# Kernel optimization log

Measured on AMD Instinct MI355X. Metric: run time of the kernel, lower is better.

Reference implementation:

```python
import jax, jax.numpy as jnp
import numpy as np
import math

D_MODEL = 1024
N_HEADS = 16
D_K = D_MODEL // N_HEADS
B, L = 4, 2048


def setup_inputs() -> dict:
    key = jax.random.key(0)
    ks = jax.random.split(key, 11)
    s = 1.0 / math.sqrt(D_MODEL)
    inp = {
        "queries": jax.random.normal(ks[0], (B, L, D_MODEL), jnp.float32),
        "keys": jax.random.normal(ks[1], (B, L, D_MODEL), jnp.float32),
        "values": jax.random.normal(ks[2], (B, L, D_MODEL), jnp.float32),
        "Wq": jax.random.normal(ks[3], (D_MODEL, D_MODEL), jnp.float32) * s,
        "bq": jax.random.normal(ks[4], (D_MODEL,), jnp.float32) * s,
        "Wk": jax.random.normal(ks[5], (D_MODEL, D_MODEL), jnp.float32) * s,
        "bk": jax.random.normal(ks[6], (D_MODEL,), jnp.float32) * s,
        "Wv": jax.random.normal(ks[7], (D_MODEL, D_MODEL), jnp.float32) * s,
        "bv": jax.random.normal(ks[8], (D_MODEL,), jnp.float32) * s,
        "Wo": jax.random.normal(ks[9], (D_MODEL, D_MODEL), jnp.float32) * s,
        "bo": jax.random.normal(ks[10], (D_MODEL,), jnp.float32) * s,
    }
    return inp


def _heads(x):
    b, l, _ = x.shape
    return x.reshape(b, l, N_HEADS, D_K).transpose(0, 2, 1, 3)  # (B,H,L,Dk)


def reference(queries, keys, values, Wq, bq, Wk, bk, Wv, bv, Wo, bo):
    Q = _heads(queries @ Wq.T + bq)
    K = _heads(keys @ Wk.T + bk)
    V = _heads(values @ Wv.T + bv)
    scores = jnp.einsum("bhqd,bhkd->bhqk", Q, K) / math.sqrt(D_K)
    t = jnp.arange(L, dtype=scores.dtype)
    time_bias = -0.1 * jnp.abs(t[None, :] - t[:, None])  # (L,L)
    attn = jax.nn.softmax(scores + time_bias[None, None], axis=-1)
    out = jnp.einsum("bhqk,bhkd->bhqd", attn, V)
    out = out.transpose(0, 2, 1, 3).reshape(queries.shape[0], L, D_MODEL)
    return out @ Wo.T + bo
```

## Files before the change

kernel.cpp:

```cpp
#include <hip/hip_runtime.h>
#include <hip/hip_bf16.h>
#include <stdint.h>

typedef __bf16 bf16x8 __attribute__((ext_vector_type(8)));
typedef float f32x4 __attribute__((ext_vector_type(4)));
typedef float f32x4v __attribute__((ext_vector_type(4)));
typedef unsigned short u16x4 __attribute__((ext_vector_type(4)));

__device__ __forceinline__ uint16_t f2bf(float f){
  __bf16 h = (__bf16)f;
  return __builtin_bit_cast(uint16_t, h);
}

__device__ __forceinline__ void gld_lds16(const void* g, void* l){
  __builtin_amdgcn_global_load_lds((const __attribute__((address_space(1))) void*)g,
                                   (__attribute__((address_space(3))) void*)l, 16, 0, 0);
}

__global__ void convert2(const float* __restrict__ s1, uint16_t* __restrict__ d1, int n4_1,
                         const float* __restrict__ s2, uint16_t* __restrict__ d2, int n4_2){
  int i = blockIdx.x * blockDim.x + threadIdx.x;
  const float* s; uint16_t* d;
  if (i < n4_1) { s = s1; d = d1; }
  else { i -= n4_1; if (i >= n4_2) return; s = s2; d = d2; }
  f32x4v v = __builtin_nontemporal_load(((const f32x4v*)s) + i);
  u16x4 o;
  o.x = f2bf(v.x); o.y = f2bf(v.y); o.z = f2bf(v.z); o.w = f2bf(v.w);
  __builtin_nontemporal_store(o, ((u16x4*)d) + i);
}

__launch_bounds__(256, 2)
__global__ void gemm_bt(const uint16_t* __restrict__ A, const uint16_t* __restrict__ W,
                        const float* __restrict__ bias, void* __restrict__ out, int mode,
                        float oscale)
{
  __shared__ uint16_t As[2][128 * 64];
  __shared__ uint16_t Ws[2][128 * 64];
  const int tid = threadIdx.x;
  const int wave = tid >> 6, lane = tid & 63;
  const int g = lane >> 4, li = lane & 15;
  const int m0 = blockIdx.x * 128, n0 = blockIdx.y * 128;
  const int wr = (wave >> 1) * 64, wc = (wave & 1) * 64;

  f32x4 acc[4][4];
#pragma unroll
  for (int m = 0; m < 4; m++)
#pragma unroll
    for (int n = 0; n < 4; n++) acc[m][n] = f32x4{0.f, 0.f, 0.f, 0.f};

  const uint16_t* Asrc[4];
  const uint16_t* Wsrc[4];
  int cid[4];
#pragma unroll
  for (int j = 0; j < 4; j++) {
    cid[j] = j * 256 + tid;
    int row = cid[j] >> 3, c = cid[j] & 7;
    int sc = c ^ (row & 7);
    Asrc[j] = A + (size_t)(m0 + row) * 1024 + sc * 8;
    Wsrc[j] = W + (size_t)(n0 + row) * 1024 + sc * 8;
  }

#pragma unroll
  for (int j = 0; j < 4; j++) {
    gld_lds16(Asrc[j], (char*)As[0] + cid[j] * 16);
    gld_lds16(Wsrc[j], (char*)Ws[0] + cid[j] * 16);
  }
  __syncthreads();

  for (int t = 0; t < 16; t++) {
    const int cur = t & 1;
    if (t < 15) {
      const int k1 = (t + 1) * 64;
      const int nxt = cur ^ 1;
#pragma unroll
      for (int j = 0; j < 4; j++) {
        gld_lds16(Asrc[j] + k1, (char*)As[nxt] + cid[j] * 16);
        gld_lds16(Wsrc[j] + k1, (char*)Ws[nxt] + cid[j] * 16);
      }
    }

    const char* Ab = (const char*)As[cur];
    const char* Wb = (const char*)Ws[cur];
#pragma unroll
    for (int kh = 0; kh < 2; kh++) {
      bf16x8 a[4], bfr[4];
#pragma unroll
      for (int m = 0; m < 4; m++) {
        int row = wr + m * 16 + li;
        int ch = (kh * 4 + g) ^ (row & 7);
        a[m] = *(const bf16x8*)(Ab + row * 128 + ch * 16);
      }
#pragma unroll
      for (int n = 0; n < 4; n++) {
        int row = wc + n * 16 + li;
        int ch = (kh * 4 + g) ^ (row & 7);
        bfr[n] = *(const bf16x8*)(Wb + row * 128 + ch * 16);
      }
#pragma unroll
      for (int m = 0; m < 4; m++)
#pragma unroll
        for (int n = 0; n < 4; n++)
          acc[m][n] = __builtin_amdgcn_mfma_f32_16x16x32_bf16(a[m], bfr[n], acc[m][n], 0, 0, 0);
    }
    __syncthreads();
  }

  if (mode == 0) {
    uint16_t* O = (uint16_t*)out;
#pragma unroll
    for (int n = 0; n < 4; n++) {
      int col = n0 + wc + n * 16 + li;
      float bv = bias[col];
#pragma unroll
      for (int m = 0; m < 4; m++) {
        int row = m0 + wr + m * 16 + g * 4;
#pragma unroll
        for (int r = 0; r < 4; r++)
          __builtin_nontemporal_store(f2bf((acc[m][n][r] + bv) * oscale),
                                      &O[(size_t)(row + r) * 1024 + col]);
      }
    }
  } else if (mode == 2) {
    uint16_t* O = (uint16_t*)out;
#pragma unroll
    for (int n = 0; n < 4; n++) {
      int col = n0 + wc + n * 16 + li;
      float bv = bias[col];
#pragma unroll
      for (int m = 0; m < 4; m++) {
        int mg = m0 + wr + m * 16 + g * 4;
        int bidx = mg >> 11;
        int l = mg & 2047;
        u16x4 pk;
        pk.x = f2bf(acc[m][n][0] + bv);
        pk.y = f2bf(acc[m][n][1] + bv);
        pk.z = f2bf(acc[m][n][2] + bv);
        pk.w = f2bf(acc[m][n][3] + bv);
        __builtin_nontemporal_store(pk,
            (u16x4*)(O + ((size_t)bidx * 1024 + col) * 2048 + l));
      }
    }
  } else {
    float* O = (float*)out;
#pragma unroll
    for (int n = 0; n < 4; n++) {
      int col = n0 + wc + n * 16 + li;
      float bv = bias[col];
#pragma unroll
      for (int m = 0; m < 4; m++) {
        int row = m0 + wr + m * 16 + g * 4;
#pragma unroll
        for (int r = 0; r < 4; r++)
          __builtin_nontemporal_store(acc[m][n][r] + bv,
                                      &O[(size_t)(row + r) * 1024 + col]);
      }
    }
  }
}

__launch_bounds__(256, 2)
__global__ void flash_attn(const uint16_t* __restrict__ Qw, const uint16_t* __restrict__ Kw,
                           const uint16_t* __restrict__ Vt, uint16_t* __restrict__ Ow)
{
  __shared__ uint16_t Ks[2][64 * 64];
  __shared__ uint16_t Vs[2][64 * 64];
  __shared__ uint16_t Ps[4][16 * 64];

  const float C2 = 0.14426950408889635f;
  const float C3 = 20.1977305724455f;

  const int tid = threadIdx.x;
  const int wave = tid >> 6, lane = tid & 63;
  const int g = lane >> 4, li = lane & 15;
  const int bh = blockIdx.x;
  const int q0 = blockIdx.y * 64;
  const int b = bh >> 4, h = bh & 15;

  const uint16_t* Qp = Qw + (size_t)(b * 2048 + q0 + wave * 16 + li) * 1024 + h * 64 + g * 8;
  bf16x8 qf0 = *(const bf16x8*)Qp;
  bf16x8 qf1 = *(const bf16x8*)(Qp + 32);

  float l_r[4] = {0.f, 0.f, 0.f, 0.f};
  f32x4 o[4];
#pragma unroll
  for (int nd = 0; nd < 4; nd++) o[nd] = f32x4{0.f, 0.f, 0.f, 0.f};

  const int cid0 = tid, cid1 = 256 + tid;
  const int kr0 = cid0 >> 3, c0 = cid0 & 7;
  const int kr1 = cid1 >> 3, c1 = cid1 & 7;
  const int sc0 = c0 ^ (kr0 & 7), sc1 = c1 ^ (kr1 & 7);

  const uint16_t* Kb0 = Kw + (size_t)(b * 2048 + kr0) * 1024 + h * 64 + sc0 * 8;
  const uint16_t* Kb1 = Kw + (size_t)(b * 2048 + kr1) * 1024 + h * 64 + sc1 * 8;
  const uint16_t* Vb0 = Vt + (size_t)(bh * 64 + kr0) * 2048 + sc0 * 8;
  const uint16_t* Vb1 = Vt + (size_t)(bh * 64 + kr1) * 2048 + sc1 * 8;

  const int kv_lo = (q0 >= 256) ? (q0 - 256) : 0;
  const int kv_hi = (q0 + 320 <= 2048) ? (q0 + 320) : 2048;
  const int ntiles = (kv_hi - kv_lo) >> 6;
  const int tq0 = q0 + wave * 16 + g * 4;

  {
    const int kv0 = kv_lo;
    gld_lds16(Kb0 + (size_t)kv0 * 1024, (char*)Ks[0] + cid0 * 16);
    gld_lds16(Kb1 + (size_t)kv0 * 1024, (char*)Ks[0] + cid1 * 16);
    gld_lds16(Vb0 + kv0, (char*)Vs[0] + cid0 * 16);
    gld_lds16(Vb1 + kv0, (char*)Vs[0] + cid1 * 16);
  }

  for (int it = 0; it < ntiles; ++it) {
    __syncthreads();
    const int cur = it & 1;
    if (it + 1 < ntiles) {
      const int kvn = kv_lo + (it + 1) * 64;
      const int nxt = cur ^ 1;
      gld_lds16(Kb0 + (size_t)kvn * 1024, (char*)Ks[nxt] + cid0 * 16);
      gld_lds16(Kb1 + (size_t)kvn * 1024, (char*)Ks[nxt] + cid1 * 16);
      gld_lds16(Vb0 + kvn, (char*)Vs[nxt] + cid0 * 16);
      gld_lds16(Vb1 + kvn, (char*)Vs[nxt] + cid1 * 16);
    }
    const int kv0 = kv_lo + it * 64;

    float p[4][4];
#pragma unroll
    for (int n = 0; n < 4; n++) {
      int kr = n * 16 + li;
      bf16x8 bk0 = *(const bf16x8*)((const char*)Ks[cur] + kr * 128 + ((g ^ (kr & 7)) << 4));
      bf16x8 bk1 = *(const bf16x8*)((const char*)Ks[cur] + kr * 128 + (((4 + g) ^ (kr & 7)) << 4));
      f32x4 s = f32x4{0.f, 0.f, 0.f, 0.f};
      s = __builtin_amdgcn_mfma_f32_16x16x32_bf16(qf0, bk0, s, 0, 0, 0);
      s = __builtin_amdgcn_mfma_f32_16x16x32_bf16(qf1, bk1, s, 0, 0, 0);
      float dtb = (float)(tq0 - (kv0 + n * 16 + li));
#pragma unroll
      for (int r = 0; r < 4; r++) {
        float e = exp2f((s[r] - C3) - C2 * fabsf(dtb + (float)r));
        p[n][r] = e;
        l_r[r] += e;
      }
    }

#pragma unroll
    for (int n = 0; n < 4; n++)
#pragma unroll
      for (int r = 0; r < 4; r++) {
        int prow = g * 4 + r;
        int c = n * 16 + li;
        Ps[wave][prow * 64 + ((((c >> 3) ^ (prow & 7))) << 3) + (c & 7)] = f2bf(p[n][r]);
      }

    bf16x8 pa0 = *(const bf16x8*)((const char*)Ps[wave] + li * 128 + ((g ^ (li & 7)) << 4));
    bf16x8 pa1 = *(const bf16x8*)((const char*)Ps[wave] + li * 128 + (((4 + g) ^ (li & 7)) << 4));
#pragma unroll
    for (int nd = 0; nd < 4; nd++) {
      int vr = nd * 16 + li;
      bf16x8 vb0 = *(const bf16x8*)((const char*)Vs[cur] + vr * 128 + ((g ^ (vr & 7)) << 4));
      bf16x8 vb1 = *(const bf16x8*)((const char*)Vs[cur] + vr * 128 + (((4 + g) ^ (vr & 7)) << 4));
      o[nd] = __builtin_amdgcn_mfma_f32_16x16x32_bf16(pa0, vb0, o[nd], 0, 0, 0);
      o[nd] = __builtin_amdgcn_mfma_f32_16x16x32_bf16(pa1, vb1, o[nd], 0, 0, 0);
    }
  }

#pragma unroll
  for (int r = 0; r < 4; r++) {
    float l = l_r[r];
    l += __shfl_xor(l, 1);
    l += __shfl_xor(l, 2);
    l += __shfl_xor(l, 4);
    l += __shfl_xor(l, 8);
    float inv = 1.0f / l;
    int qg = b * 2048 + q0 + wave * 16 + g * 4 + r;
#pragma unroll
    for (int nd = 0; nd < 4; nd++)
      __builtin_nontemporal_store(f2bf(o[nd][r] * inv),
                                  &Ow[(size_t)qg * 1024 + h * 64 + nd * 16 + li]);
  }
}

extern "C" void kernel_launch(void* const* d_in, const int* in_sizes, int n_in,
                              void* d_out, int out_size, void* d_ws, size_t ws_size,
                              hipStream_t stream) {
  const float* q  = (const float*)d_in[0];
  const float* k  = (const float*)d_in[1];
  const float* v  = (const float*)d_in[2];
  const float* Wq = (const float*)d_in[3];
  const float* bq = (const float*)d_in[4];
  const float* Wk = (const float*)d_in[5];
  const float* bk = (const float*)d_in[6];
  const float* Wv = (const float*)d_in[7];
  const float* bv = (const float*)d_in[8];
  const float* Wo = (const float*)d_in[9];
  const float* bo = (const float*)d_in[10];

  const size_t NX = (size_t)8192 * 1024;
  const size_t NW = (size_t)1024 * 1024;

  uint16_t* Xb  = (uint16_t*)d_ws;
  uint16_t* Wb  = Xb + NX;
  uint16_t* Vtw = Wb + NW;
  uint16_t* Aws = Xb;
  uint16_t* Qws = (uint16_t*)d_out;
  uint16_t* Kws = Qws + NX;

  const int n4x = (int)(NX / 4);
  const int n4w = (int)(NW / 4);
  const int gcv = (n4x + n4w) / 256;

  dim3 ggrid(64, 8);
  const float qscale = 0.18033688011112042f;

  convert2<<<gcv, 256, 0, stream>>>(q, Xb, n4x, Wq, Wb, n4w);
  gemm_bt<<<ggrid, 256, 0, stream>>>(Xb, Wb, bq, Qws, 0, qscale);

  convert2<<<gcv, 256, 0, stream>>>(k, Xb, n4x, Wk, Wb, n4w);
  gemm_bt<<<ggrid, 256, 0, stream>>>(Xb, Wb, bk, Kws, 0, 1.0f);

  convert2<<<gcv, 256, 0, stream>>>(v, Xb, n4x, Wv, Wb, n4w);
  gemm_bt<<<ggrid, 256, 0, stream>>>(Xb, Wb, bv, Vtw, 2, 1.0f);

  flash_attn<<<dim3(64, 32), 256, 0, stream>>>(Qws, Kws, Vtw, Aws);

  convert2<<<n4w / 256, 256, 0, stream>>>(Wo, Wb, n4w, (const float*)0, (uint16_t*)0, 0);
  gemm_bt<<<ggrid, 256, 0, stream>>>(Aws, Wb, bo, d_out, 3, 1.0f);
}
```

Before: 346.3 us.

## Transpose QK^T MFMA and pass P via lane shuffles instead of LDS

The flash attention kernel swaps the QK^T MFMA operands so each lane holds scores for one query row. It packs the exp'd probabilities into bf16 pairs and assembles the PV A-operand with cross-lane shuffles, removing the per-wave Ps shared-memory round trip. The row-sum reduction is restructured to match. Separately, nontemporal loads and stores are replaced with plain ones across the convert, GEMM and attention kernels. Shuffles add ds_bpermute traffic in exchange for dropping LDS writes and reads.

```diff
diff --git a/kernel.cpp b/kernel.cpp
--- a/kernel.cpp
+++ b/kernel.cpp
@@ -4,12 +4,14 @@
 
 typedef __bf16 bf16x8 __attribute__((ext_vector_type(8)));
 typedef float f32x4 __attribute__((ext_vector_type(4)));
-typedef float f32x4v __attribute__((ext_vector_type(4)));
-typedef unsigned short u16x4 __attribute__((ext_vector_type(4)));
+typedef uint32_t u32x4 __attribute__((ext_vector_type(4)));
 
 __device__ __forceinline__ uint16_t f2bf(float f){
   __bf16 h = (__bf16)f;
   return __builtin_bit_cast(uint16_t, h);
+}
+__device__ __forceinline__ uint32_t pkbf(float lo, float hi){
+  return (uint32_t)f2bf(lo) | ((uint32_t)f2bf(hi) << 16);
 }
 
 __device__ __forceinline__ void gld_lds16(const void* g, void* l){
@@ -23,10 +25,10 @@
   const float* s; uint16_t* d;
   if (i < n4_1) { s = s1; d = d1; }
   else { i -= n4_1; if (i >= n4_2) return; s = s2; d = d2; }
-  f32x4v v = __builtin_nontemporal_load(((const f32x4v*)s) + i);
-  u16x4 o;
+  float4 v = ((const float4*)s)[i];
+  ushort4 o;
   o.x = f2bf(v.x); o.y = f2bf(v.y); o.z = f2bf(v.z); o.w = f2bf(v.w);
-  __builtin_nontemporal_store(o, ((u16x4*)d) + i);
+  ((ushort4*)d)[i] = o;
 }
 
 __launch_bounds__(256, 2)
@@ -116,8 +118,7 @@
         int row = m0 + wr + m * 16 + g * 4;
 #pragma unroll
         for (int r = 0; r < 4; r++)
-          __builtin_nontemporal_store(f2bf((acc[m][n][r] + bv) * oscale),
-                                      &O[(size_t)(row + r) * 1024 + col]);
+          O[(size_t)(row + r) * 1024 + col] = f2bf((acc[m][n][r] + bv) * oscale);
       }
     }
   } else if (mode == 2) {
@@ -131,13 +132,12 @@
         int mg = m0 + wr + m * 16 + g * 4;
         int bidx = mg >> 11;
         int l = mg & 2047;
-        u16x4 pk;
+        ushort4 pk;
         pk.x = f2bf(acc[m][n][0] + bv);
         pk.y = f2bf(acc[m][n][1] + bv);
         pk.z = f2bf(acc[m][n][2] + bv);
         pk.w = f2bf(acc[m][n][3] + bv);
-        __builtin_nontemporal_store(pk,
-            (u16x4*)(O + ((size_t)bidx * 1024 + col) * 2048 + l));
+        *(ushort4*)(O + ((size_t)bidx * 1024 + col) * 2048 + l) = pk;
       }
     }
   } else {
@@ -151,8 +151,7 @@
         int row = m0 + wr + m * 16 + g * 4;
 #pragma unroll
         for (int r = 0; r < 4; r++)
-          __builtin_nontemporal_store(acc[m][n][r] + bv,
-                                      &O[(size_t)(row + r) * 1024 + col]);
+          O[(size_t)(row + r) * 1024 + col] = acc[m][n][r] + bv;
       }
     }
   }
@@ -164,7 +163,6 @@
 {
   __shared__ uint16_t Ks[2][64 * 64];
   __shared__ uint16_t Vs[2][64 * 64];
-  __shared__ uint16_t Ps[4][16 * 64];
 
   const float C2 = 0.14426950408889635f;
   const float C3 = 20.1977305724455f;
@@ -180,7 +178,7 @@
   bf16x8 qf0 = *(const bf16x8*)Qp;
   bf16x8 qf1 = *(const bf16x8*)(Qp + 32);
 
-  float l_r[4] = {0.f, 0.f, 0.f, 0.f};
+  float l_own = 0.f;
   f32x4 o[4];
 #pragma unroll
   for (int nd = 0; nd < 4; nd++) o[nd] = f32x4{0.f, 0.f, 0.f, 0.f};
@@ -198,15 +196,15 @@
   const int kv_lo = (q0 >= 256) ? (q0 - 256) : 0;
   const int kv_hi = (q0 + 320 <= 2048) ? (q0 + 320) : 2048;
   const int ntiles = (kv_hi - kv_lo) >> 6;
-  const int tq0 = q0 + wave * 16 + g * 4;
-
-  {
-    const int kv0 = kv_lo;
-    gld_lds16(Kb0 + (size_t)kv0 * 1024, (char*)Ks[0] + cid0 * 16);
-    gld_lds16(Kb1 + (size_t)kv0 * 1024, (char*)Ks[0] + cid1 * 16);
-    gld_lds16(Vb0 + kv0, (char*)Vs[0] + cid0 * 16);
-    gld_lds16(Vb1 + kv0, (char*)Vs[0] + cid1 * 16);
-  }
+  const int tq = q0 + wave * 16 + li;
+  const int sA = li + 32 * (g & 1);
+  const int sB = sA + 16;
+  const bool gsel = (g < 2);
+
+  gld_lds16(Kb0 + (size_t)kv_lo * 1024, (char*)Ks[0] + cid0 * 16);
+  gld_lds16(Kb1 + (size_t)kv_lo * 1024, (char*)Ks[0] + cid1 * 16);
+  gld_lds16(Vb0 + kv_lo, (char*)Vs[0] + cid0 * 16);
+  gld_lds16(Vb1 + kv_lo, (char*)Vs[0] + cid1 * 16);
 
   for (int it = 0; it < ntiles; ++it) {
     __syncthreads();
@@ -221,35 +219,43 @@
     }
     const int kv0 = kv_lo + it * 64;
 
-    float p[4][4];
+    uint32_t w0[4], w1[4];
 #pragma unroll
     for (int n = 0; n < 4; n++) {
       int kr = n * 16 + li;
       bf16x8 bk0 = *(const bf16x8*)((const char*)Ks[cur] + kr * 128 + ((g ^ (kr & 7)) << 4));
       bf16x8 bk1 = *(const bf16x8*)((const char*)Ks[cur] + kr * 128 + (((4 + g) ^ (kr & 7)) << 4));
       f32x4 s = f32x4{0.f, 0.f, 0.f, 0.f};
-      s = __builtin_amdgcn_mfma_f32_16x16x32_bf16(qf0, bk0, s, 0, 0, 0);
-      s = __builtin_amdgcn_mfma_f32_16x16x32_bf16(qf1, bk1, s, 0, 0, 0);
-      float dtb = (float)(tq0 - (kv0 + n * 16 + li));
-#pragma unroll
-      for (int r = 0; r < 4; r++) {
-        float e = exp2f((s[r] - C3) - C2 * fabsf(dtb + (float)r));
-        p[n][r] = e;
-        l_r[r] += e;
-      }
-    }
-
-#pragma unroll
-    for (int n = 0; n < 4; n++)
-#pragma unroll
-      for (int r = 0; r < 4; r++) {
-        int prow = g * 4 + r;
-        int c = n * 16 + li;
-        Ps[wave][prow * 64 + ((((c >> 3) ^ (prow & 7))) << 3) + (c & 7)] = f2bf(p[n][r]);
-      }
-
-    bf16x8 pa0 = *(const bf16x8*)((const char*)Ps[wave] + li * 128 + ((g ^ (li & 7)) << 4));
-    bf16x8 pa1 = *(const bf16x8*)((const char*)Ps[wave] + li * 128 + (((4 + g) ^ (li & 7)) << 4));
+      s = __builtin_amdgcn_mfma_f32_16x16x32_bf16(bk0, qf0, s, 0, 0, 0);
+      s = __builtin_amdgcn_mfma_f32_16x16x32_bf16(bk1, qf1, s, 0, 0, 0);
+      float dtb = (float)(tq - (kv0 + n * 16 + g * 4));
+      float p0 = exp2f((s[0] - C3) - C2 * fabsf(dtb));
+      float p1 = exp2f((s[1] - C3) - C2 * fabsf(dtb - 1.f));
+      float p2 = exp2f((s[2] - C3) - C2 * fabsf(dtb - 2.f));
+      float p3 = exp2f((s[3] - C3) - C2 * fabsf(dtb - 3.f));
+      l_own += (p0 + p1) + (p2 + p3);
+      w0[n] = pkbf(p0, p1);
+      w1[n] = pkbf(p2, p3);
+    }
+
+    u32x4 pa0u, pa1u;
+    {
+      uint32_t a0 = __shfl((int)w0[0], sA), b0 = __shfl((int)w0[1], sA);
+      uint32_t a1 = __shfl((int)w1[0], sA), b1 = __shfl((int)w1[1], sA);
+      uint32_t a2 = __shfl((int)w0[0], sB), b2 = __shfl((int)w0[1], sB);
+      uint32_t a3 = __shfl((int)w1[0], sB), b3 = __shfl((int)w1[1], sB);
+      pa0u.x = gsel ? a0 : b0;  pa0u.y = gsel ? a1 : b1;
+      pa0u.z = gsel ? a2 : b2;  pa0u.w = gsel ? a3 : b3;
+      uint32_t c0_ = __shfl((int)w0[2], sA), d0 = __shfl((int)w0[3], sA);
+      uint32_t c1_ = __shfl((int)w1[2], sA), d1 = __shfl((int)w1[3], sA);
+      uint32_t c2_ = __shfl((int)w0[2], sB), d2 = __shfl((int)w0[3], sB);
+      uint32_t c3_ = __shfl((int)w1[2], sB), d3 = __shfl((int)w1[3], sB);
+      pa1u.x = gsel ? c0_ : d0;  pa1u.y = gsel ? c1_ : d1;
+      pa1u.z = gsel ? c2_ : d2;  pa1u.w = gsel ? c3_ : d3;
+    }
+    bf16x8 pa0 = __builtin_bit_cast(bf16x8, pa0u);
+    bf16x8 pa1 = __builtin_bit_cast(bf16x8, pa1u);
+
 #pragma unroll
     for (int nd = 0; nd < 4; nd++) {
       int vr = nd * 16 + li;
@@ -260,19 +266,18 @@
     }
   }
 
+  float l_full = l_own;
+  l_full += __shfl_xor(l_full, 16);
+  l_full += __shfl_xor(l_full, 32);
+
 #pragma unroll
   for (int r = 0; r < 4; r++) {
-    float l = l_r[r];
-    l += __shfl_xor(l, 1);
-    l += __shfl_xor(l, 2);
-    l += __shfl_xor(l, 4);
-    l += __shfl_xor(l, 8);
-    float inv = 1.0f / l;
+    float lr = __shfl(l_full, (lane & 48) | (g * 4 + r));
+    float inv = 1.0f / lr;
     int qg = b * 2048 + q0 + wave * 16 + g * 4 + r;
 #pragma unroll
     for (int nd = 0; nd < 4; nd++)
-      __builtin_nontemporal_store(f2bf(o[nd][r] * inv),
-                                  &Ow[(size_t)qg * 1024 + h * 64 + nd * 16 + li]);
+      Ow[(size_t)qg * 1024 + h * 64 + nd * 16 + li] = f2bf(o[nd][r] * inv);
   }
 }
 
```

After: 309.0 us. -10.8%, faster.
